# Optimization experiments

Measured on AMD Instinct MI355X. Metric: run time of the kernel, lower is better.

Reference implementation:

```python
import jax, jax.numpy as jnp
import numpy as np

B, N, E = 2, 2048, 1024
H, D = 16, 64


def setup_inputs() -> dict:
    key = jax.random.key(0)
    k1, k2, k3 = jax.random.split(key, 3)
    x = jax.random.normal(k1, (B, N, E), dtype=jnp.float32)
    Wqkv = jax.random.normal(k2, (3 * H * D, E), dtype=jnp.float32) * 0.02
    bqkv = jnp.zeros((3 * H * D,), dtype=jnp.float32)
    Wout = jax.random.normal(k3, (E, H * D), dtype=jnp.float32) * 0.02
    bout = jnp.zeros((E,), dtype=jnp.float32)
    return {"x": x, "Wqkv": Wqkv, "bqkv": bqkv, "Wout": Wout, "bout": bout}


def reference(x, Wqkv, bqkv, Wout, bout):
    b, n, _ = x.shape
    scale = D ** (-0.5)
    # qkv projection: [b, n, 3*h*d], interpreted as (h, d, qkv) per einops pattern
    qkv = (x @ Wqkv.T + bqkv).reshape(b, n, H, D, 3)
    q = jnp.transpose(qkv[..., 0], (0, 2, 1, 3))  # [b, h, n, d]
    k = jnp.transpose(qkv[..., 1], (0, 2, 1, 3))
    v = jnp.transpose(qkv[..., 2], (0, 2, 1, 3))
    att = jnp.einsum('bhid,bhjd->bhij', q, k) * scale  # [b, h, n, n]
    causal = jnp.tril(jnp.ones((n, n), dtype=bool))
    att = jnp.where(causal, att, -jnp.inf)
    att = jax.nn.softmax(att, axis=-1)
    out = jnp.einsum('bhij,bhjd->bhid', att, v)  # [b, h, n, d]
    out = jnp.transpose(out, (0, 2, 1, 3)).reshape(b, n, H * D)
    return out @ Wout.T + bout
```

## Files before the change

kernel.cpp:

```cpp
#include <hip/hip_runtime.h>
#include <hip/hip_bf16.h>

#define B_ 2
#define N_ 2048
#define E_ 1024
#define H_ 16
#define D_ 64
#define M_ 4096
#define HD_ 1024
#define NT_ 3072

using f32x4  = __attribute__((ext_vector_type(4))) float;
using f32x16 = __attribute__((ext_vector_type(16))) float;
using bf16x8 = __attribute__((ext_vector_type(8))) short;

static __device__ __forceinline__ unsigned short f2bf(float f) {
  union { float f; unsigned u; } v; v.f = f;
  unsigned r = v.u + 0x7FFF + ((v.u >> 16) & 1);
  return (unsigned short)(r >> 16);
}
static __device__ __forceinline__ float bf2f(short s) {
  union { unsigned u; float f; } v; v.u = ((unsigned)(unsigned short)s) << 16; return v.f;
}

static __device__ __forceinline__ void gld16(const void* g, void* l) {
  __builtin_amdgcn_global_load_lds(
      (const __attribute__((address_space(1))) unsigned int*)g,
      (__attribute__((address_space(3))) unsigned int*)l, 16, 0, 0);
}

static __device__ __forceinline__ unsigned cvtpk(float lo, float hi) {
  unsigned r;
  asm("v_cvt_pk_bf16_f32 %0, %1, %2" : "=v"(r) : "v"(lo), "v"(hi));
  return r;
}
static __device__ __forceinline__ void pl32swap(unsigned& a, unsigned& b) {
  asm("v_permlane32_swap_b32 %0, %1" : "+v"(a), "+v"(b));
}

static __device__ __forceinline__ int gswz(int row) {
  return ((row >> 1) & 3) ^ ((row >> 3) & 1);
}


__global__ void k_cvt_x(const float* __restrict__ x, unsigned short* __restrict__ xb) {
  int t = blockIdx.x * 256 + threadIdx.x;
  float4 v = reinterpret_cast<const float4*>(x)[t];
  ushort4 o;
  o.x = f2bf(v.x); o.y = f2bf(v.y); o.z = f2bf(v.z); o.w = f2bf(v.w);
  reinterpret_cast<ushort4*>(xb)[t] = o;
}

__global__ void k_cvt_wqkv(const float* __restrict__ w, const float* __restrict__ bsrc,
                           unsigned short* __restrict__ wb, float* __restrict__ br) {
  int t = blockIdx.x * 256 + threadIdx.x;
  int r = t >> 8;
  int c = (t & 255) * 4;
  int kind = r >> 10, hd = r & 1023;
  int h = hd >> 6, d = hd & 63;
  int rin = h * 192 + d * 3 + kind;
  float s = (kind == 0) ? 0.125f * 1.4426950408889634f : 1.0f;
  float4 v = *reinterpret_cast<const float4*>(w + (size_t)rin * E_ + c);
  ushort4 o;
  o.x = f2bf(v.x * s); o.y = f2bf(v.y * s); o.z = f2bf(v.z * s); o.w = f2bf(v.w * s);
  *reinterpret_cast<ushort4*>(wb + (size_t)r * E_ + c) = o;
  if (c == 0) br[r] = bsrc[rin] * s;
}

__global__ void k_cvt_wout(const float* __restrict__ w, unsigned short* __restrict__ wb) {
  int t = blockIdx.x * 256 + threadIdx.x;
  int r = t >> 8;
  int c = (t & 255) * 4;
  float4 v = *reinterpret_cast<const float4*>(w + (size_t)r * HD_ + c);
  ushort4 o;
  o.x = f2bf(v.x); o.y = f2bf(v.y); o.z = f2bf(v.z); o.w = f2bf(v.w);
  *reinterpret_cast<ushort4*>(wb + (size_t)r * HD_ + c) = o;
}

template <int EPI, int BM>
__global__ __launch_bounds__(256, 2) void k_gemm(
    const unsigned short* __restrict__ A,
    const unsigned short* __restrict__ W,
    const float* __restrict__ bias,
    unsigned short* __restrict__ Qo, unsigned short* __restrict__ Ko,
    unsigned short* __restrict__ Vo, float* __restrict__ Fo,
    int M, int Nt, int K)
{
  constexpr int APT = (BM == 128) ? 2 : 1;
  constexpr int LPI = APT + 2;
  constexpr int NF  = (BM == 128) ? 4 : 2;
  constexpr int ASZ = 3 * BM * 32;
  constexpr int MAIN_B = (ASZ + 3 * 128 * 32) * 2;
  constexpr int EPI_B  = (EPI == 0) ? 128 * 136 * 2 : 64 * 132 * 4;
  constexpr int SMB = MAIN_B > EPI_B ? MAIN_B : EPI_B;
  __shared__ alignas(16) char smem[SMB];
  unsigned short* AsBase = (unsigned short*)smem;
  unsigned short* BsBase = AsBase + ASZ;

  const int t = threadIdx.x;
  const int w = t >> 6, l = t & 63, lg = l >> 4, lr = l & 15;
  const int wrow0 = (BM == 128) ? (w >> 1) * 64 : 0;
  const int wcol0 = (BM == 128) ? (w & 1) * 64 : w * 32;
  const int row0 = blockIdx.x * BM, col0 = blockIdx.y * 128;
  const int NT = K >> 5;

  f32x4 acc[4][NF] = {};

  auto stage = [&](int b, int k0) {
#pragma unroll
    for (int c = 0; c < APT; ++c) {
      int ci = w * APT + c;
      int row = ci * 16 + (l >> 2);
      int sub = (l & 3) ^ gswz(row);
      gld16(A + (size_t)(row0 + row) * K + k0 + sub * 8, AsBase + b * BM * 32 + ci * 512);
    }
#pragma unroll
    for (int c = 0; c < 2; ++c) {
      int ci = w * 2 + c;
      int row = ci * 16 + (l >> 2);
      int sub = (l & 3) ^ gswz(row);
      gld16(W + (size_t)(col0 + row) * K + k0 + sub * 8, BsBase + b * 128 * 32 + ci * 512);
    }
  };

  stage(0, 0);
  stage(1, 32);

  for (int kt = 0; kt < NT; ++kt) {
    const int ib = kt % 3;
    if (kt + 2 < NT) stage((kt + 2) % 3, (kt + 2) * 32);
    const int na = NT - 1 - kt;
    if (na >= 2) {
      if constexpr (LPI == 4) asm volatile("s_waitcnt vmcnt(8)" ::: "memory");
      else                    asm volatile("s_waitcnt vmcnt(6)" ::: "memory");
    } else if (na == 1) {
      if constexpr (LPI == 4) asm volatile("s_waitcnt vmcnt(4)" ::: "memory");
      else                    asm volatile("s_waitcnt vmcnt(3)" ::: "memory");
    } else {
      asm volatile("s_waitcnt vmcnt(0)" ::: "memory");
    }
    asm volatile("s_barrier" ::: "memory");

    bf16x8 af[4], bf[NF];
#pragma unroll
    for (int m = 0; m < 4; ++m) {
      int row = wrow0 + m * 16 + lr;
      af[m] = *reinterpret_cast<const bf16x8*>(
          &AsBase[ib * BM * 32 + row * 32 + ((lg ^ gswz(row)) * 8)]);
    }
#pragma unroll
    for (int n = 0; n < NF; ++n) {
      int row = wcol0 + n * 16 + lr;
      bf[n] = *reinterpret_cast<const bf16x8*>(
          &BsBase[ib * 128 * 32 + row * 32 + ((lg ^ gswz(row)) * 8)]);
    }
    __builtin_amdgcn_s_setprio(1);
#pragma unroll
    for (int m = 0; m < 4; ++m)
#pragma unroll
      for (int n = 0; n < NF; ++n)
        acc[m][n] = __builtin_amdgcn_mfma_f32_16x16x32_bf16(af[m], bf[n], acc[m][n], 0, 0, 0);
    __builtin_amdgcn_s_setprio(0);

    asm volatile("s_barrier" ::: "memory");
  }

  if (EPI == 0) {
    const int kind = col0 >> 10;
    if (kind < 2) {
      unsigned short* eb = (unsigned short*)smem;
#pragma unroll
      for (int m = 0; m < 4; ++m)
#pragma unroll
        for (int n = 0; n < NF; ++n) {
          int c = wcol0 + n * 16 + lr;
          float bb = bias[col0 + c];
#pragma unroll
          for (int rr = 0; rr < 4; ++rr)
            eb[(wrow0 + m * 16 + lg * 4 + rr) * 136 + c] = f2bf(acc[m][n][rr] + bb);
        }
      __syncthreads();
      unsigned short* outp = kind ? Ko : Qo;
      int h0 = (col0 & 1023) >> 6;
      int row = t >> 1, cs = (t & 1) * 64;
      int ro = row0 + row;
      int bi = ro >> 11, ni = ro & 2047;
#pragma unroll
      for (int j = 0; j < 8; ++j) {
        int c = cs + j * 8;
        int h = h0 + (c >> 6), d = c & 63;
        bf16x8 v = *reinterpret_cast<const bf16x8*>(&eb[row * 136 + c]);
        *reinterpret_cast<bf16x8*>(
            &outp[((size_t)(bi * H_ + h) * N_ + ni) * D_ + d]) = v;
      }
    } else {
#pragma unroll
      for (int m = 0; m < 4; ++m)
#pragma unroll
        for (int n = 0; n < NF; ++n) {
          int hd = (col0 + wcol0 + n * 16 + lr) & 1023;
          int h = hd >> 6, d = hd & 63;
          float bb = bias[col0 + wcol0 + n * 16 + lr];
          int ro = row0 + wrow0 + m * 16 + lg * 4;
          int bi = ro >> 11, ni = ro & 2047;
          ushort4 pk;
          pk.x = f2bf(acc[m][n][0] + bb);
          pk.y = f2bf(acc[m][n][1] + bb);
          pk.z = f2bf(acc[m][n][2] + bb);
          pk.w = f2bf(acc[m][n][3] + bb);
          *reinterpret_cast<ushort4*>(
              &Vo[((size_t)(bi * H_ + h) * D_ + d) * N_ + ni]) = pk;
        }
    }
  } else {
    float* ef = (float*)smem;
#pragma unroll
    for (int m = 0; m < 4; ++m)
#pragma unroll
      for (int n = 0; n < NF; ++n) {
        int c = wcol0 + n * 16 + lr;
        float bb = bias[col0 + c];
#pragma unroll
        for (int rr = 0; rr < 4; ++rr)
          ef[(m * 16 + lg * 4 + rr) * 132 + c] = acc[m][n][rr] + bb;
      }
    __syncthreads();
    int row = t >> 2, cs = (t & 3) * 32;
#pragma unroll
    for (int j = 0; j < 8; ++j) {
      float4 v = *reinterpret_cast<const float4*>(&ef[row * 132 + cs + j * 4]);
      *reinterpret_cast<float4*>(
          &Fo[(size_t)(row0 + row) * HD_ + col0 + cs + j * 4]) = v;
    }
  }
}

__global__ __launch_bounds__(256, 3) void k_attn(
    const unsigned short* __restrict__ Q,
    const unsigned short* __restrict__ Kg,
    const unsigned short* __restrict__ Vg,
    unsigned short* __restrict__ O,
    unsigned short* __restrict__ Pp,
    float* __restrict__ Pml)
{
  static const int u_qt[24] = {15,15,14,13,12,11,10, 9,   8, 7,14, 6,13, 5,12, 4,   8, 0, 9, 1,10, 2,11, 3};
  static const int u_t0[24] = { 0,16, 0, 0, 0, 0, 0, 0,   0, 0,16, 0,16, 0,16, 0,  16, 0,16, 0,16, 0,16, 0};
  static const int u_ps[24] = {14,15,12,10, 8, 6, 4, 2,   0,-1,13,-1,11,-1, 9,-1,   1,-1, 3,-1, 5,-1, 7,-1};

  __shared__ alignas(16) unsigned short Ks[3][64 * 64];
  __shared__ alignas(16) unsigned short Vs[3][64 * 64];

  const int t = threadIdx.x;
  const int w = t >> 6, l = t & 63;
  const int lq = l & 31;
  const int hi = l >> 5;
  const int bh = blockIdx.x & 31;
  const int u  = blockIdx.x >> 5;
  const int qt = u_qt[u], t0 = u_t0[u], ps = u_ps[u];
  const int q0 = qt * 128;
  const int r0w = q0 + w * 32;
  const int rtop = r0w + 31;
  const bool splitc0 = (ps >= 0) && (t0 == 0);
  const int tendW = splitc0 ? 16 : ((rtop >> 6) + 1);
  const int tendB = splitc0 ? 16 : (((q0 + 127) >> 6) + 1);

  const unsigned short* Qb = Q  + (size_t)bh * (N_ * D_);
  const unsigned short* Kb = Kg + (size_t)bh * (N_ * D_);
  const unsigned short* Vb = Vg + (size_t)bh * (N_ * D_);

  const int pr  = l >> 3;
  const int pswz = ((l & 7) ^ pr) * 8;
  const unsigned short* KsrcB = Kb + pr * D_ + pswz;
  const unsigned short* VsrcB = Vb + pr * N_ + pswz;

  bf16x8 qf[4];
#pragma unroll
  for (int ks = 0; ks < 4; ++ks)
    qf[ks] = *reinterpret_cast<const bf16x8*>(
        Qb + (size_t)(r0w + lq) * D_ + ks * 16 + hi * 8);

  f32x16 oacc[2] = {};
  float lrun = 0.f;

  auto stage = [&](int b, int kt_) {
    const int kv = kt_ * 64;
#pragma unroll
    for (int c = 0; c < 2; ++c) {
      int cb = w * 2 + c;
      gld16(KsrcB + kv * D_ + cb * 512, (unsigned short*)&Ks[b][0] + cb * 512);
      gld16(VsrcB + kv + cb * 8 * N_,   (unsigned short*)&Vs[b][0] + cb * 512);
    }
  };

  auto read_kf = [&](int b, bf16x8 kf[2][4]) {
#pragma unroll
    for (int ct = 0; ct < 2; ++ct)
#pragma unroll
      for (int ks = 0; ks < 4; ++ks) {
        int row = ct * 32 + lq;
        kf[ct][ks] = *reinterpret_cast<const bf16x8*>(
            &Ks[b][row * 64 + (((ks * 2 + hi) ^ (lq & 7)) * 8)]);
      }
  };

  stage(0, t0);
  stage(1, t0 + 1);
  asm volatile("s_waitcnt vmcnt(4)" ::: "memory");
  __syncthreads();

  f32x16 scur[2];
  {
    bf16x8 kf[2][4];
    read_kf(0, kf);
#pragma unroll
    for (int ct = 0; ct < 2; ++ct) {
      f32x16 z = {};
#pragma unroll
      for (int ks = 0; ks < 4; ++ks)
        z = __builtin_amdgcn_mfma_f32_32x32x16_bf16(kf[ct][ks], qf[ks], z, 0, 0, 0);
      scur[ct] = z;
    }
  }

  for (int kt = t0; kt < tendB; ++kt) {
    const int ib  = (kt - t0) % 3;
    const int ib1 = (kt - t0 + 1) % 3;
    if (kt + 2 < tendB) {
      stage((kt - t0 + 2) % 3, kt + 2);
      asm volatile("s_waitcnt vmcnt(4)" ::: "memory");
    } else {
      asm volatile("s_waitcnt vmcnt(0)" ::: "memory");
    }
    asm volatile("s_barrier" ::: "memory");

    bf16x8 kf[2][4];
    read_kf(ib1, kf);
    f32x16 snext[2];
#pragma unroll
    for (int ct = 0; ct < 2; ++ct) {
      f32x16 z = {};
#pragma unroll
      for (int ks = 0; ks < 4; ++ks)
        z = __builtin_amdgcn_mfma_f32_32x32x16_bf16(kf[ct][ks], qf[ks], z, 0, 0, 0);
      snext[ct] = z;
    }

    if (kt < tendW) {
      const int kv0 = kt * 64;
      if (kv0 + 63 > r0w) {
        int qrow = r0w + lq;
#pragma unroll
        for (int ct = 0; ct < 2; ++ct)
#pragma unroll
          for (int r = 0; r < 16; ++r) {
            int kv = kv0 + ct * 32 + (r & 3) + 8 * (r >> 2) + 4 * hi;
            if (kv > qrow) scur[ct][r] = -1e30f;
          }
      }

      float s16[16];
#pragma unroll
      for (int r = 0; r < 16; ++r) {
        float p0 = exp2f(scur[0][r]);
        float p1 = exp2f(scur[1][r]);
        scur[0][r] = p0; scur[1][r] = p1;
        s16[r] = p0 + p1;
      }
#pragma unroll
      for (int st = 8; st >= 1; st >>= 1)
#pragma unroll
        for (int r = 0; r < 8; ++r)
          if (r < st) s16[r] += s16[r + st];
      lrun += s16[0] + __shfl_xor(s16[0], 32);

      bf16x8 paf[4];
#pragma unroll
      for (int ct = 0; ct < 2; ++ct) {
        unsigned u0 = cvtpk(scur[ct][0],  scur[ct][1]);
        unsigned u1 = cvtpk(scur[ct][2],  scur[ct][3]);
        unsigned u2 = cvtpk(scur[ct][4],  scur[ct][5]);
        unsigned u3 = cvtpk(scur[ct][6],  scur[ct][7]);
        unsigned u4 = cvtpk(scur[ct][8],  scur[ct][9]);
        unsigned u5 = cvtpk(scur[ct][10], scur[ct][11]);
        unsigned u6 = cvtpk(scur[ct][12], scur[ct][13]);
        unsigned u7 = cvtpk(scur[ct][14], scur[ct][15]);
        pl32swap(u0, u2); pl32swap(u1, u3);
        pl32swap(u4, u6); pl32swap(u5, u7);
        union { unsigned uu[4]; bf16x8 v; } c0, c1;
        c0.uu[0] = u0; c0.uu[1] = u1; c0.uu[2] = u2; c0.uu[3] = u3;
        c1.uu[0] = u4; c1.uu[1] = u5; c1.uu[2] = u6; c1.uu[3] = u7;
        paf[ct * 2]     = c0.v;
        paf[ct * 2 + 1] = c1.v;
      }

      bf16x8 vf[2][4];
#pragma unroll
      for (int dt = 0; dt < 2; ++dt)
#pragma unroll
        for (int j = 0; j < 4; ++j) {
          int row = dt * 32 + lq;
          vf[dt][j] = *reinterpret_cast<const bf16x8*>(
              &Vs[ib][row * 64 + (((j * 2 + hi) ^ (lq & 7)) * 8)]);
        }
      __builtin_amdgcn_s_setprio(1);
#pragma unroll
      for (int dt = 0; dt < 2; ++dt)
#pragma unroll
        for (int j = 0; j < 4; ++j)
          oacc[dt] = __builtin_amdgcn_mfma_f32_32x32x16_bf16(paf[j], vf[dt][j], oacc[dt], 0, 0, 0);
      __builtin_amdgcn_s_setprio(0);
    }

    scur[0] = snext[0];
    scur[1] = snext[1];
    asm volatile("s_barrier" ::: "memory");
  }

  int bi = bh >> 4, h = bh & 15;
  float scale = (ps < 0) ? (1.0f / lrun) : 1.0f;
  float iv[16];
#pragma unroll
  for (int r = 0; r < 16; ++r)
    iv[r] = __shfl(scale, (r & 3) + 8 * (r >> 2) + 4 * hi);
  unsigned short* eb = (unsigned short*)&Ks[0][0];
#pragma unroll
  for (int dt = 0; dt < 2; ++dt)
#pragma unroll
    for (int r = 0; r < 16; ++r) {
      int rloc = w * 32 + (r & 3) + 8 * (r >> 2) + 4 * hi;
      eb[rloc * 72 + dt * 32 + lq] = f2bf(oacc[dt][r] * iv[r]);
    }
  if (ps >= 0 && l < 32)
    Pml[(size_t)(bh * 16 + ps) * 128 + w * 32 + l] = lrun;
  __syncthreads();
  int rl = t >> 1, dsg = (t & 1) * 32;
  if (ps < 0) {
    int qr = q0 + rl;
    unsigned short* op = O + ((size_t)(bi * N_ + qr) * H_ + h) * D_ + dsg;
#pragma unroll
    for (int j = 0; j < 4; ++j)
      *reinterpret_cast<bf16x8*>(op + j * 8) =
          *reinterpret_cast<const bf16x8*>(&eb[rl * 72 + dsg + j * 8]);
  } else {
    unsigned short* pb = Pp + (size_t)(bh * 16 + ps) * (128 * 64) + rl * 64 + dsg;
#pragma unroll
    for (int j = 0; j < 4; ++j)
      *reinterpret_cast<bf16x8*>(pb + j * 8) =
          *reinterpret_cast<const bf16x8*>(&eb[rl * 72 + dsg + j * 8]);
  }
}

__global__ void k_merge(const unsigned short* __restrict__ Pp,
                        const float* __restrict__ Pml,
                        unsigned short* __restrict__ O) {
  int t = blockIdx.x * 256 + threadIdx.x;
  int dseg = t & 7;
  int rloc = (t >> 3) & 127;
  int qt8 = (t >> 10) & 7;
  int bh  = t >> 13;
  size_t b0 = (size_t)(bh * 16 + qt8 * 2) * 128 + rloc;
  size_t b1 = b0 + 128;
  bf16x8 o0 = *reinterpret_cast<const bf16x8*>(Pp + b0 * 64 + dseg * 8);
  bf16x8 o1 = *reinterpret_cast<const bf16x8*>(Pp + b1 * 64 + dseg * 8);
  float l0 = Pml[b0], l1 = Pml[b1];
  float inv = 1.0f / (l0 + l1);
  int n = (qt8 + 8) * 128 + rloc;
  int bi = bh >> 4, h = bh & 15;
  unsigned short* op = O + ((size_t)(bi * N_ + n) * H_ + h) * D_ + dseg * 8;
  bf16x8 res;
#pragma unroll
  for (int j = 0; j < 8; ++j)
    res[j] = (short)f2bf((bf2f(o0[j]) + bf2f(o1[j])) * inv);
  *reinterpret_cast<bf16x8*>(op) = res;
}


extern "C" void kernel_launch(void* const* d_in, const int* in_sizes, int n_in,
                              void* d_out, int out_size, void* d_ws, size_t ws_size,
                              hipStream_t stream) {
  const float* x    = (const float*)d_in[0];
  const float* Wqkv = (const float*)d_in[1];
  const float* bqkv = (const float*)d_in[2];
  const float* Wout = (const float*)d_in[3];
  const float* bout = (const float*)d_in[4];
  float* out = (float*)d_out;

  char* ws = (char*)d_ws;
  unsigned short* xb  = (unsigned short*)ws; ws += (size_t)M_ * E_ * 2;
  unsigned short* wqb = (unsigned short*)ws; ws += (size_t)NT_ * E_ * 2;
  float*          bqr = (float*)ws;          ws += 16384;
  unsigned short* wob = (unsigned short*)ws; ws += (size_t)E_ * HD_ * 2;
  unsigned short* Qb  = (unsigned short*)ws; ws += (size_t)M_ * D_ * H_ * 2;
  unsigned short* Kb  = (unsigned short*)ws; ws += (size_t)M_ * D_ * H_ * 2;
  unsigned short* Vb  = (unsigned short*)ws; ws += (size_t)M_ * D_ * H_ * 2;
  unsigned short* ao  = (unsigned short*)ws; ws += (size_t)M_ * HD_ * 2;

  unsigned short* Pp  = xb;
  float*          Pml = (float*)wqb;

  k_cvt_x<<<(M_ * E_) / 4 / 256, 256, 0, stream>>>(x, xb);
  k_cvt_wqkv<<<NT_, 256, 0, stream>>>(Wqkv, bqkv, wqb, bqr);
  k_cvt_wout<<<E_, 256, 0, stream>>>(Wout, wob);

  k_gemm<0, 128><<<dim3(M_ / 128, NT_ / 128), 256, 0, stream>>>(
      xb, wqb, bqr, Qb, Kb, Vb, nullptr, M_, NT_, E_);

  k_attn<<<768, 256, 0, stream>>>(Qb, Kb, Vb, ao, Pp, Pml);
  k_merge<<<1024, 256, 0, stream>>>(Pp, Pml, ao);

  k_gemm<1, 64><<<dim3(M_ / 64, HD_ / 128), 256, 0, stream>>>(
      ao, wob, bout, nullptr, nullptr, nullptr, out, M_, HD_, E_);
}
```

Before: 119.3 us.

## Rebalance causal attention work with finer KV splits and fuse conversion kernels

Replaces the attention work schedule with a new table in which each block processes one or two segments. Long query tiles are split into up to three KV chunks, and short tiles are paired with long ones, to even out per-block work across the causal triangle. The QK^T software pipelining (computing next scores early) is dropped in favour of a simpler per-tile loop. Output is now written directly from registers instead of staged through shared memory, and partial results go to a transposed scratch layout that the reworked merge kernel combines over 2 or 3 chunks. The three conversion kernels are fused into one launch, and the merge kernel's strided reads and the loss of score prefetch could cost some time.

```diff
diff --git a/kernel.cpp b/kernel.cpp
--- a/kernel.cpp
+++ b/kernel.cpp
@@ -42,39 +42,39 @@
   return ((row >> 1) & 3) ^ ((row >> 3) & 1);
 }
 
-
-__global__ void k_cvt_x(const float* __restrict__ x, unsigned short* __restrict__ xb) {
-  int t = blockIdx.x * 256 + threadIdx.x;
-  float4 v = reinterpret_cast<const float4*>(x)[t];
-  ushort4 o;
-  o.x = f2bf(v.x); o.y = f2bf(v.y); o.z = f2bf(v.z); o.w = f2bf(v.w);
-  reinterpret_cast<ushort4*>(xb)[t] = o;
-}
-
-__global__ void k_cvt_wqkv(const float* __restrict__ w, const float* __restrict__ bsrc,
-                           unsigned short* __restrict__ wb, float* __restrict__ br) {
-  int t = blockIdx.x * 256 + threadIdx.x;
-  int r = t >> 8;
-  int c = (t & 255) * 4;
-  int kind = r >> 10, hd = r & 1023;
-  int h = hd >> 6, d = hd & 63;
-  int rin = h * 192 + d * 3 + kind;
-  float s = (kind == 0) ? 0.125f * 1.4426950408889634f : 1.0f;
-  float4 v = *reinterpret_cast<const float4*>(w + (size_t)rin * E_ + c);
-  ushort4 o;
-  o.x = f2bf(v.x * s); o.y = f2bf(v.y * s); o.z = f2bf(v.z * s); o.w = f2bf(v.w * s);
-  *reinterpret_cast<ushort4*>(wb + (size_t)r * E_ + c) = o;
-  if (c == 0) br[r] = bsrc[rin] * s;
-}
-
-__global__ void k_cvt_wout(const float* __restrict__ w, unsigned short* __restrict__ wb) {
-  int t = blockIdx.x * 256 + threadIdx.x;
-  int r = t >> 8;
-  int c = (t & 255) * 4;
-  float4 v = *reinterpret_cast<const float4*>(w + (size_t)r * HD_ + c);
-  ushort4 o;
-  o.x = f2bf(v.x); o.y = f2bf(v.y); o.z = f2bf(v.z); o.w = f2bf(v.w);
-  *reinterpret_cast<ushort4*>(wb + (size_t)r * HD_ + c) = o;
+__global__ void k_cvt(const float* __restrict__ x, unsigned short* __restrict__ xb,
+                      const float* __restrict__ wq, const float* __restrict__ bsrc,
+                      unsigned short* __restrict__ wqb, float* __restrict__ br,
+                      const float* __restrict__ wo, unsigned short* __restrict__ wob) {
+  int b = blockIdx.x;
+  if (b < 4096) {
+    int t = b * 256 + threadIdx.x;
+    float4 v = reinterpret_cast<const float4*>(x)[t];
+    ushort4 o;
+    o.x = f2bf(v.x); o.y = f2bf(v.y); o.z = f2bf(v.z); o.w = f2bf(v.w);
+    reinterpret_cast<ushort4*>(xb)[t] = o;
+  } else if (b < 7168) {
+    int t = (b - 4096) * 256 + threadIdx.x;
+    int r = t >> 8;
+    int c = (t & 255) * 4;
+    int kind = r >> 10, hd = r & 1023;
+    int h = hd >> 6, d = hd & 63;
+    int rin = h * 192 + d * 3 + kind;
+    float s = (kind == 0) ? 0.125f * 1.4426950408889634f : 1.0f;
+    float4 v = *reinterpret_cast<const float4*>(wq + (size_t)rin * E_ + c);
+    ushort4 o;
+    o.x = f2bf(v.x * s); o.y = f2bf(v.y * s); o.z = f2bf(v.z * s); o.w = f2bf(v.w * s);
+    *reinterpret_cast<ushort4*>(wqb + (size_t)r * E_ + c) = o;
+    if (c == 0) br[r] = bsrc[rin] * s;
+  } else {
+    int t = (b - 7168) * 256 + threadIdx.x;
+    int r = t >> 8;
+    int c = (t & 255) * 4;
+    float4 v = *reinterpret_cast<const float4*>(wo + (size_t)r * HD_ + c);
+    ushort4 o;
+    o.x = f2bf(v.x); o.y = f2bf(v.y); o.z = f2bf(v.z); o.w = f2bf(v.w);
+    *reinterpret_cast<ushort4*>(wob + (size_t)r * HD_ + c) = o;
+  }
 }
 
 template <int EPI, int BM>
@@ -243,9 +243,13 @@
     unsigned short* __restrict__ Pp,
     float* __restrict__ Pml)
 {
-  static const int u_qt[24] = {15,15,14,13,12,11,10, 9,   8, 7,14, 6,13, 5,12, 4,   8, 0, 9, 1,10, 2,11, 3};
-  static const int u_t0[24] = { 0,16, 0, 0, 0, 0, 0, 0,   0, 0,16, 0,16, 0,16, 0,  16, 0,16, 0,16, 0,16, 0};
-  static const int u_ps[24] = {14,15,12,10, 8, 6, 4, 2,   0,-1,13,-1,11,-1, 9,-1,   1,-1, 3,-1, 5,-1, 7,-1};
+  static const int u_qtA[24] = {15,15,15,14,14,14,13,13,13,12,12,12,11,11,11,10,10, 5, 9, 9, 6, 8, 8, 7};
+  static const int u_t0A[24] = { 0,12,23, 0,12,23, 0,12,23, 0,12,23, 0,12,23, 0,12, 1, 0,12, 3, 0,12, 5};
+  static const int u_teA[24] = {12,23,32,12,23,30,12,23,28,12,23,26,12,23,24,12,22,12,12,20,14,12,18,16};
+  static const int u_psA[24] = { 0, 1, 2, 3, 4, 5, 6, 7, 8, 9,10,11,12,13,14,15,16,26,17,18,24,19,20,22};
+  static const int u_qtB[24] = {-1,-1, 0,-1,-1, 1,-1,-1, 2,-1,-1, 3,-1,-1, 4,-1, 5,-1,-1, 6,-1,-1, 7,-1};
+  static const int u_teB[24] = { 0, 0, 2, 0, 0, 4, 0, 0, 6, 0, 0, 8, 0, 0,10, 0, 1, 0, 0, 3, 0, 0, 5, 0};
+  static const int u_psB[24] = { 0, 0,-1, 0, 0,-1, 0, 0,-1, 0, 0,-1, 0, 0,-1, 0,25, 0, 0,23, 0, 0,21, 0};
 
   __shared__ alignas(16) unsigned short Ks[3][64 * 64];
   __shared__ alignas(16) unsigned short Vs[3][64 * 64];
@@ -256,13 +260,6 @@
   const int hi = l >> 5;
   const int bh = blockIdx.x & 31;
   const int u  = blockIdx.x >> 5;
-  const int qt = u_qt[u], t0 = u_t0[u], ps = u_ps[u];
-  const int q0 = qt * 128;
-  const int r0w = q0 + w * 32;
-  const int rtop = r0w + 31;
-  const bool splitc0 = (ps >= 0) && (t0 == 0);
-  const int tendW = splitc0 ? 16 : ((rtop >> 6) + 1);
-  const int tendB = splitc0 ? 16 : (((q0 + 127) >> 6) + 1);
 
   const unsigned short* Qb = Q  + (size_t)bh * (N_ * D_);
   const unsigned short* Kb = Kg + (size_t)bh * (N_ * D_);
@@ -272,15 +269,7 @@
   const int pswz = ((l & 7) ^ pr) * 8;
   const unsigned short* KsrcB = Kb + pr * D_ + pswz;
   const unsigned short* VsrcB = Vb + pr * N_ + pswz;
-
-  bf16x8 qf[4];
-#pragma unroll
-  for (int ks = 0; ks < 4; ++ks)
-    qf[ks] = *reinterpret_cast<const bf16x8*>(
-        Qb + (size_t)(r0w + lq) * D_ + ks * 16 + hi * 8);
-
-  f32x16 oacc[2] = {};
-  float lrun = 0.f;
+  const int bi = bh >> 4, h = bh & 15;
 
   auto stage = [&](int b, int kt_) {
     const int kv = kt_ * 64;
@@ -292,161 +281,162 @@
     }
   };
 
-  auto read_kf = [&](int b, bf16x8 kf[2][4]) {
-#pragma unroll
-    for (int ct = 0; ct < 2; ++ct)
-#pragma unroll
-      for (int ks = 0; ks < 4; ++ks) {
-        int row = ct * 32 + lq;
-        kf[ct][ks] = *reinterpret_cast<const bf16x8*>(
-            &Ks[b][row * 64 + (((ks * 2 + hi) ^ (lq & 7)) * 8)]);
+  for (int seg = 0; seg < 2; ++seg) {
+    const int qt = (seg == 0) ? u_qtA[u] : u_qtB[u];
+    if (qt < 0) break;
+    const int t0 = (seg == 0) ? u_t0A[u] : 0;
+    const int te = (seg == 0) ? u_teA[u] : u_teB[u];
+    const int ps = (seg == 0) ? u_psA[u] : u_psB[u];
+    const int q0 = qt * 128;
+    const int r0w = q0 + w * 32;
+    const int rtop = r0w + 31;
+    const int tendW = min(te, (rtop >> 6) + 1);
+
+    bf16x8 qf[4];
+#pragma unroll
+    for (int ks = 0; ks < 4; ++ks)
+      qf[ks] = *reinterpret_cast<const bf16x8*>(
+          Qb + (size_t)(r0w + lq) * D_ + ks * 16 + hi * 8);
+
+    f32x16 oacc[2] = {};
+    float lrun = 0.f;
+
+    stage(0, t0);
+    stage(1, t0 + 1);
+    asm volatile("s_waitcnt vmcnt(4)" ::: "memory");
+    asm volatile("s_barrier" ::: "memory");
+
+    for (int kt = t0; kt < te; ++kt) {
+      const int ib = (kt - t0) % 3;
+      if (kt + 2 < te) stage((kt - t0 + 2) % 3, kt + 2);
+      const int na = te - 1 - kt;
+      if (na >= 2)      asm volatile("s_waitcnt vmcnt(8)" ::: "memory");
+      else if (na == 1) asm volatile("s_waitcnt vmcnt(4)" ::: "memory");
+      else              asm volatile("s_waitcnt vmcnt(0)" ::: "memory");
+      asm volatile("s_barrier" ::: "memory");
+
+      if (kt < tendW) {
+        const int kv0 = kt * 64;
+        bf16x8 kf[2][4], vf[2][4];
+#pragma unroll
+        for (int ct = 0; ct < 2; ++ct)
+#pragma unroll
+          for (int ks = 0; ks < 4; ++ks) {
+            int row = ct * 32 + lq;
+            kf[ct][ks] = *reinterpret_cast<const bf16x8*>(
+                &Ks[ib][row * 64 + (((ks * 2 + hi) ^ (lq & 7)) * 8)]);
+          }
+#pragma unroll
+        for (int dt = 0; dt < 2; ++dt)
+#pragma unroll
+          for (int j = 0; j < 4; ++j) {
+            int row = dt * 32 + lq;
+            vf[dt][j] = *reinterpret_cast<const bf16x8*>(
+                &Vs[ib][row * 64 + (((j * 2 + hi) ^ (lq & 7)) * 8)]);
+          }
+
+        f32x16 sct[2];
+        __builtin_amdgcn_s_setprio(1);
+#pragma unroll
+        for (int ct = 0; ct < 2; ++ct) {
+          f32x16 z = {};
+#pragma unroll
+          for (int ks = 0; ks < 4; ++ks)
+            z = __builtin_amdgcn_mfma_f32_32x32x16_bf16(kf[ct][ks], qf[ks], z, 0, 0, 0);
+          sct[ct] = z;
+        }
+        __builtin_amdgcn_s_setprio(0);
+
+        if (kv0 + 63 > r0w) {
+          int qrow = r0w + lq;
+#pragma unroll
+          for (int ct = 0; ct < 2; ++ct)
+#pragma unroll
+            for (int r = 0; r < 16; ++r) {
+              int kv = kv0 + ct * 32 + (r & 3) + 8 * (r >> 2) + 4 * hi;
+              if (kv > qrow) sct[ct][r] = -1e30f;
+            }
+        }
+
+        float s16[16];
+#pragma unroll
+        for (int r = 0; r < 16; ++r) {
+          float p0 = exp2f(sct[0][r]);
+          float p1 = exp2f(sct[1][r]);
+          sct[0][r] = p0; sct[1][r] = p1;
+          s16[r] = p0 + p1;
+        }
+#pragma unroll
+        for (int st = 8; st >= 1; st >>= 1)
+#pragma unroll
+          for (int r = 0; r < 8; ++r)
+            if (r < st) s16[r] += s16[r + st];
+        lrun += s16[0] + __shfl_xor(s16[0], 32);
+
+        bf16x8 paf[4];
+#pragma unroll
+        for (int ct = 0; ct < 2; ++ct) {
+          unsigned u0 = cvtpk(sct[ct][0],  sct[ct][1]);
+          unsigned u1 = cvtpk(sct[ct][2],  sct[ct][3]);
+          unsigned u2 = cvtpk(sct[ct][4],  sct[ct][5]);
+          unsigned u3 = cvtpk(sct[ct][6],  sct[ct][7]);
+          unsigned u4 = cvtpk(sct[ct][8],  sct[ct][9]);
+          unsigned u5 = cvtpk(sct[ct][10], sct[ct][11]);
+          unsigned u6 = cvtpk(sct[ct][12], sct[ct][13]);
+          unsigned u7 = cvtpk(sct[ct][14], sct[ct][15]);
+          pl32swap(u0, u2); pl32swap(u1, u3);
+          pl32swap(u4, u6); pl32swap(u5, u7);
+          union { unsigned uu[4]; bf16x8 v; } c0, c1;
+          c0.uu[0] = u0; c0.uu[1] = u1; c0.uu[2] = u2; c0.uu[3] = u3;
+          c1.uu[0] = u4; c1.uu[1] = u5; c1.uu[2] = u6; c1.uu[3] = u7;
+          paf[ct * 2]     = c0.v;
+          paf[ct * 2 + 1] = c1.v;
+        }
+
+        __builtin_amdgcn_s_setprio(1);
+#pragma unroll
+        for (int dt = 0; dt < 2; ++dt)
+#pragma unroll
+          for (int j = 0; j < 4; ++j)
+            oacc[dt] = __builtin_amdgcn_mfma_f32_32x32x16_bf16(paf[j], vf[dt][j], oacc[dt], 0, 0, 0);
+        __builtin_amdgcn_s_setprio(0);
       }
-  };
-
-  stage(0, t0);
-  stage(1, t0 + 1);
-  asm volatile("s_waitcnt vmcnt(4)" ::: "memory");
-  __syncthreads();
-
-  f32x16 scur[2];
-  {
-    bf16x8 kf[2][4];
-    read_kf(0, kf);
-#pragma unroll
-    for (int ct = 0; ct < 2; ++ct) {
-      f32x16 z = {};
-#pragma unroll
-      for (int ks = 0; ks < 4; ++ks)
-        z = __builtin_amdgcn_mfma_f32_32x32x16_bf16(kf[ct][ks], qf[ks], z, 0, 0, 0);
-      scur[ct] = z;
-    }
-  }
-
-  for (int kt = t0; kt < tendB; ++kt) {
-    const int ib  = (kt - t0) % 3;
-    const int ib1 = (kt - t0 + 1) % 3;
-    if (kt + 2 < tendB) {
-      stage((kt - t0 + 2) % 3, kt + 2);
-      asm volatile("s_waitcnt vmcnt(4)" ::: "memory");
+
+      asm volatile("s_barrier" ::: "memory");
+    }
+
+    if (ps >= 0) {
+      const int slot = bh * 27 + ps;
+      unsigned short* pb = Pp + (size_t)slot * 8192;
+#pragma unroll
+      for (int dt = 0; dt < 2; ++dt) {
+        int d = dt * 32 + lq;
+#pragma unroll
+        for (int g = 0; g < 4; ++g) {
+          ushort4 pk;
+          pk.x = f2bf(oacc[dt][g * 4 + 0]);
+          pk.y = f2bf(oacc[dt][g * 4 + 1]);
+          pk.z = f2bf(oacc[dt][g * 4 + 2]);
+          pk.w = f2bf(oacc[dt][g * 4 + 3]);
+          *reinterpret_cast<ushort4*>(&pb[d * 128 + w * 32 + 8 * g + 4 * hi]) = pk;
+        }
+      }
+      if (l < 32) Pml[(size_t)slot * 128 + w * 32 + l] = lrun;
     } else {
-      asm volatile("s_waitcnt vmcnt(0)" ::: "memory");
-    }
-    asm volatile("s_barrier" ::: "memory");
-
-    bf16x8 kf[2][4];
-    read_kf(ib1, kf);
-    f32x16 snext[2];
-#pragma unroll
-    for (int ct = 0; ct < 2; ++ct) {
-      f32x16 z = {};
-#pragma unroll
-      for (int ks = 0; ks < 4; ++ks)
-        z = __builtin_amdgcn_mfma_f32_32x32x16_bf16(kf[ct][ks], qf[ks], z, 0, 0, 0);
-      snext[ct] = z;
-    }
-
-    if (kt < tendW) {
-      const int kv0 = kt * 64;
-      if (kv0 + 63 > r0w) {
-        int qrow = r0w + lq;
-#pragma unroll
-        for (int ct = 0; ct < 2; ++ct)
-#pragma unroll
-          for (int r = 0; r < 16; ++r) {
-            int kv = kv0 + ct * 32 + (r & 3) + 8 * (r >> 2) + 4 * hi;
-            if (kv > qrow) scur[ct][r] = -1e30f;
-          }
-      }
-
-      float s16[16];
-#pragma unroll
-      for (int r = 0; r < 16; ++r) {
-        float p0 = exp2f(scur[0][r]);
-        float p1 = exp2f(scur[1][r]);
-        scur[0][r] = p0; scur[1][r] = p1;
-        s16[r] = p0 + p1;
-      }
-#pragma unroll
-      for (int st = 8; st >= 1; st >>= 1)
-#pragma unroll
-        for (int r = 0; r < 8; ++r)
-          if (r < st) s16[r] += s16[r + st];
-      lrun += s16[0] + __shfl_xor(s16[0], 32);
-
-      bf16x8 paf[4];
-#pragma unroll
-      for (int ct = 0; ct < 2; ++ct) {
-        unsigned u0 = cvtpk(scur[ct][0],  scur[ct][1]);
-        unsigned u1 = cvtpk(scur[ct][2],  scur[ct][3]);
-        unsigned u2 = cvtpk(scur[ct][4],  scur[ct][5]);
-        unsigned u3 = cvtpk(scur[ct][6],  scur[ct][7]);
-        unsigned u4 = cvtpk(scur[ct][8],  scur[ct][9]);
-        unsigned u5 = cvtpk(scur[ct][10], scur[ct][11]);
-        unsigned u6 = cvtpk(scur[ct][12], scur[ct][13]);
-        unsigned u7 = cvtpk(scur[ct][14], scur[ct][15]);
-        pl32swap(u0, u2); pl32swap(u1, u3);
-        pl32swap(u4, u6); pl32swap(u5, u7);
-        union { unsigned uu[4]; bf16x8 v; } c0, c1;
-        c0.uu[0] = u0; c0.uu[1] = u1; c0.uu[2] = u2; c0.uu[3] = u3;
-        c1.uu[0] = u4; c1.uu[1] = u5; c1.uu[2] = u6; c1.uu[3] = u7;
-        paf[ct * 2]     = c0.v;
-        paf[ct * 2 + 1] = c1.v;
-      }
-
-      bf16x8 vf[2][4];
+      float inv = 1.0f / lrun;
+      float iv[16];
+#pragma unroll
+      for (int r = 0; r < 16; ++r)
+        iv[r] = __shfl(inv, (r & 3) + 8 * (r >> 2) + 4 * hi);
 #pragma unroll
       for (int dt = 0; dt < 2; ++dt)
 #pragma unroll
-        for (int j = 0; j < 4; ++j) {
-          int row = dt * 32 + lq;
-          vf[dt][j] = *reinterpret_cast<const bf16x8*>(
-              &Vs[ib][row * 64 + (((j * 2 + hi) ^ (lq & 7)) * 8)]);
-        }
-      __builtin_amdgcn_s_setprio(1);
-#pragma unroll
-      for (int dt = 0; dt < 2; ++dt)
-#pragma unroll
-        for (int j = 0; j < 4; ++j)
-          oacc[dt] = __builtin_amdgcn_mfma_f32_32x32x16_bf16(paf[j], vf[dt][j], oacc[dt], 0, 0, 0);
-      __builtin_amdgcn_s_setprio(0);
-    }
-
-    scur[0] = snext[0];
-    scur[1] = snext[1];
-    asm volatile("s_barrier" ::: "memory");
-  }
-
-  int bi = bh >> 4, h = bh & 15;
-  float scale = (ps < 0) ? (1.0f / lrun) : 1.0f;
-  float iv[16];
-#pragma unroll
-  for (int r = 0; r < 16; ++r)
-    iv[r] = __shfl(scale, (r & 3) + 8 * (r >> 2) + 4 * hi);
-  unsigned short* eb = (unsigned short*)&Ks[0][0];
-#pragma unroll
-  for (int dt = 0; dt < 2; ++dt)
-#pragma unroll
-    for (int r = 0; r < 16; ++r) {
-      int rloc = w * 32 + (r & 3) + 8 * (r >> 2) + 4 * hi;
-      eb[rloc * 72 + dt * 32 + lq] = f2bf(oacc[dt][r] * iv[r]);
-    }
-  if (ps >= 0 && l < 32)
-    Pml[(size_t)(bh * 16 + ps) * 128 + w * 32 + l] = lrun;
-  __syncthreads();
-  int rl = t >> 1, dsg = (t & 1) * 32;
-  if (ps < 0) {
-    int qr = q0 + rl;
-    unsigned short* op = O + ((size_t)(bi * N_ + qr) * H_ + h) * D_ + dsg;
-#pragma unroll
-    for (int j = 0; j < 4; ++j)
-      *reinterpret_cast<bf16x8*>(op + j * 8) =
-          *reinterpret_cast<const bf16x8*>(&eb[rl * 72 + dsg + j * 8]);
-  } else {
-    unsigned short* pb = Pp + (size_t)(bh * 16 + ps) * (128 * 64) + rl * 64 + dsg;
-#pragma unroll
-    for (int j = 0; j < 4; ++j)
-      *reinterpret_cast<bf16x8*>(pb + j * 8) =
-          *reinterpret_cast<const bf16x8*>(&eb[rl * 72 + dsg + j * 8]);
+        for (int r = 0; r < 16; ++r) {
+          int qr = r0w + (r & 3) + 8 * (r >> 2) + 4 * hi;
+          int d = dt * 32 + lq;
+          O[((size_t)(bi * N_ + qr) * H_ + h) * D_ + d] = f2bf(oacc[dt][r] * iv[r]);
+        }
+    }
   }
 }
 
@@ -456,22 +446,30 @@
   int t = blockIdx.x * 256 + threadIdx.x;
   int dseg = t & 7;
   int rloc = (t >> 3) & 127;
-  int qt8 = (t >> 10) & 7;
-  int bh  = t >> 13;
-  size_t b0 = (size_t)(bh * 16 + qt8 * 2) * 128 + rloc;
-  size_t b1 = b0 + 128;
-  bf16x8 o0 = *reinterpret_cast<const bf16x8*>(Pp + b0 * 64 + dseg * 8);
-  bf16x8 o1 = *reinterpret_cast<const bf16x8*>(Pp + b1 * 64 + dseg * 8);
-  float l0 = Pml[b0], l1 = Pml[b1];
-  float inv = 1.0f / (l0 + l1);
-  int n = (qt8 + 8) * 128 + rloc;
+  int r = t >> 10;
+  int qtj = r % 11;
+  int bh  = r / 11;
+  int qt = 5 + qtj;
+  int nch = (qt >= 11) ? 3 : 2;
+  int base = (qt >= 11) ? (15 - qt) * 3 : 25 - (qt - 5) * 2;
+  int s0 = bh * 27 + base;
+  float lt = 0.f;
+  float acc[8] = {};
+  for (int c = 0; c < nch; ++c) {
+    int s = s0 + c;
+    lt += Pml[(size_t)s * 128 + rloc];
+    const unsigned short* pp = Pp + (size_t)s * 8192;
+#pragma unroll
+    for (int j = 0; j < 8; ++j)
+      acc[j] += bf2f((short)pp[(dseg * 8 + j) * 128 + rloc]);
+  }
+  float inv = 1.0f / lt;
+  int n = qt * 128 + rloc;
   int bi = bh >> 4, h = bh & 15;
-  unsigned short* op = O + ((size_t)(bi * N_ + n) * H_ + h) * D_ + dseg * 8;
   bf16x8 res;
 #pragma unroll
-  for (int j = 0; j < 8; ++j)
-    res[j] = (short)f2bf((bf2f(o0[j]) + bf2f(o1[j])) * inv);
-  *reinterpret_cast<bf16x8*>(op) = res;
+  for (int j = 0; j < 8; ++j) res[j] = (short)f2bf(acc[j] * inv);
+  *reinterpret_cast<bf16x8*>(O + ((size_t)(bi * N_ + n) * H_ + h) * D_ + dseg * 8) = res;
 }
 
 
@@ -496,17 +494,15 @@
   unsigned short* ao  = (unsigned short*)ws; ws += (size_t)M_ * HD_ * 2;
 
   unsigned short* Pp  = xb;
-  float*          Pml = (float*)wqb;
-
-  k_cvt_x<<<(M_ * E_) / 4 / 256, 256, 0, stream>>>(x, xb);
-  k_cvt_wqkv<<<NT_, 256, 0, stream>>>(Wqkv, bqkv, wqb, bqr);
-  k_cvt_wout<<<E_, 256, 0, stream>>>(Wout, wob);
+  float*          Pml = (float*)(xb + (size_t)864 * 8192);
+
+  k_cvt<<<8192, 256, 0, stream>>>(x, xb, Wqkv, bqkv, wqb, bqr, Wout, wob);
 
   k_gemm<0, 128><<<dim3(M_ / 128, NT_ / 128), 256, 0, stream>>>(
       xb, wqb, bqr, Qb, Kb, Vb, nullptr, M_, NT_, E_);
 
   k_attn<<<768, 256, 0, stream>>>(Qb, Kb, Vb, ao, Pp, Pml);
-  k_merge<<<1024, 256, 0, stream>>>(Pp, Pml, ao);
+  k_merge<<<1408, 256, 0, stream>>>(Pp, Pml, ao);
 
   k_gemm<1, 64><<<dim3(M_ / 64, HD_ / 128), 256, 0, stream>>>(
       ao, wob, bout, nullptr, nullptr, nullptr, out, M_, HD_, E_);
```

Measured after the change: 121.0 us. Within noise of the previous version (+1.4%).
